# Kernel optimization log

Measured on AMD Instinct MI355X. Metric: run time of the kernel, lower is better.

Reference implementation:

```python
import jax, jax.numpy as jnp
from jax import lax
import numpy as np

BN_EPS = 1e-5

def _bn(x, g, b, m, v):
    # inference-mode BatchNorm1d (running stats)
    return (x - m) * (g / jnp.sqrt(v + BN_EPS)) + b

def _mlp2(x, W1, g, b, m, v, W2):
    # Linear(no bias) -> BN -> ReLU -> (Dropout off in eval) -> Linear(no bias)
    h = jax.nn.relu(_bn(x @ W1.T, g, b, m, v))
    return h @ W2.T

def setup_inputs() -> dict:
    key = jax.random.key(0)
    ks = iter(jax.random.split(key, 40))
    B, N = 1024, 10
    f32 = jnp.float32
    def w(shape, s=0.02):
        return jax.random.normal(next(ks), shape, f32) * s
    def bn_params(c):
        return (jnp.ones((c,), f32), jnp.zeros((c,), f32),
                jax.random.normal(next(ks), (c,), f32) * 0.1,
                jax.random.uniform(next(ks), (c,), f32, 0.5, 1.5))
    inp = {
        'features_object': jax.random.normal(next(ks), (B, N, 1024), f32),
        'bbox': jax.random.uniform(next(ks), (B, N, 4), f32),
        'word_embedding': jax.random.normal(next(ks), (B, N, 300), f32),
        'sentiment': jax.random.normal(next(ks), (B, N, 4096), f32),
        'body': jax.random.normal(next(ks), (B, 2048), f32),
    }
    # mlp_object: 1024 -> 128 -> 128
    inp['W1_o'] = w((128, 1024)); inp['g_o'], inp['b_o'], inp['m_o'], inp['v_o'] = bn_params(128)
    inp['W2_o'] = w((128, 128))
    # mlp_sentiment: 4096 -> 512 -> 128
    inp['W1_s'] = w((512, 4096)); inp['g_s'], inp['b_s'], inp['m_s'], inp['v_s'] = bn_params(512)
    inp['W2_s'] = w((128, 512))
    # mlp_body: 2048 -> 256 -> 128
    inp['W1_b'] = w((256, 2048)); inp['g_b'], inp['b_b'], inp['m_b'], inp['v_b'] = bn_params(256)
    inp['W2_b'] = w((128, 256))
    # channel attention (CBAM-style, in_planes=10, ratio=2): shared MLP 10->5->10
    inp['Wc1'] = w((5, 10), 0.3)
    inp['Wc2'] = w((10, 5), 0.3)
    # spatial attention: Conv1d(2 -> 1, k=7, pad=3, no bias)
    inp['Wsa'] = w((1, 2, 7), 0.3)
    # fc1: 688 -> 256 (with bias) then BN
    inp['Wf'] = w((256, 688)); inp['bf'] = jnp.zeros((256,), f32)
    inp['g_f'], inp['b_f'], inp['m_f'], inp['v_f'] = bn_params(256)
    return inp

def reference(features_object, bbox, word_embedding, sentiment, body,
              W1_o, g_o, b_o, m_o, v_o, W2_o,
              W1_s, g_s, b_s, m_s, v_s, W2_s,
              W1_b, g_b, b_b, m_b, v_b, W2_b,
              Wc1, Wc2, Wsa, Wf, bf, g_f, b_f, m_f, v_f):
    B, N, _ = features_object.shape
    # per-slice MLPs batched into single GEMMs over B*N rows
    obj = _mlp2(features_object.reshape(B * N, -1), W1_o, g_o, b_o, m_o, v_o, W2_o).reshape(B, N, 128)
    sen = _mlp2(sentiment.reshape(B * N, -1), W1_s, g_s, b_s, m_s, v_s, W2_s).reshape(B, N, 128)
    # body is identical across the N repeats (inference BN), compute once and broadcast
    bod = _mlp2(body.reshape(B, -1), W1_b, g_b, b_b, m_b, v_b, W2_b)
    bod = jnp.broadcast_to(bod[:, None, :], (B, N, 128))
    x = jnp.concatenate([obj, bbox, word_embedding, sen, bod], axis=2)  # [B,N,688]
    # channel attention over the N-slice axis
    def ca_mlp(a):  # [B,N] -> [B,N]
        return jax.nn.relu(a @ Wc1.T) @ Wc2.T
    att_c = jax.nn.sigmoid(ca_mlp(x.mean(axis=2)) + ca_mlp(x.max(axis=2)))  # [B,N]
    x = x * att_c[:, :, None]
    # spatial attention along feature axis
    s = jnp.stack([x.mean(axis=1), x.max(axis=1)], axis=1)  # [B,2,688]
    sa = lax.conv_general_dilated(s, Wsa, (1,), [(3, 3)],
                                  dimension_numbers=('NCH', 'OIH', 'NCH'))  # [B,1,688]
    x = x * jax.nn.sigmoid(sa)
    x = x.sum(axis=1)  # [B,688]
    out = jax.nn.relu(_bn(x @ Wf.T + bf, g_f, b_f, m_f, v_f))  # [B,256]
    return out
```

## Files before the change

kernel.cpp:

```cpp
#include <hip/hip_runtime.h>
#include <hip/hip_bf16.h>
#include <math.h>

typedef __attribute__((ext_vector_type(8))) short short8;
typedef __attribute__((ext_vector_type(4))) float floatx4;

static __device__ __forceinline__ unsigned short f2bf(float f) {
    unsigned int u = __float_as_uint(f);
    unsigned int r = (u + 0x7fffu + ((u >> 16) & 1u)) >> 16;
    return (unsigned short)r;
}

static __device__ __forceinline__ void g2l16(const void* g, void* l) {
    __builtin_amdgcn_global_load_lds(
        (const __attribute__((address_space(1))) unsigned int*)g,
        (__attribute__((address_space(3))) unsigned int*)l,
        16, 0, 0);
}

struct GDesc {
    const float*          Af;
    const unsigned short* Ab;
    const unsigned short* W;
    float*          Cf;
    unsigned short* Cb;
    const float *bias, *g, *b, *m, *v;
    int M, N, K;
    int Kreal;
    int fuse;
    int nbx;
    int block0;
};
struct GArgs { GDesc g[3]; int n; };

__global__ __launch_bounds__(256)
void gemm_grouped(GArgs ga)
{
    __shared__ unsigned short As[2][4096];
    __shared__ unsigned short Bs[2][4096];

    const int bid = blockIdx.x;
    int gi = 0;
    #pragma unroll
    for (int i = 1; i < 3; ++i)
        if (i < ga.n && bid >= ga.g[i].block0) gi = i;
    const GDesc d = ga.g[gi];
    const int local = bid - d.block0;
    const int bx = local % d.nbx;
    const int by = local / d.nbx;
    const int row0 = by * 128;
    const int col0 = bx * 128;

    const int tid  = threadIdx.x;
    const int wave = tid >> 6;
    const int lane = tid & 63;
    const int qd   = lane >> 4;
    const int ln   = lane & 15;
    const int wr   = (wave >> 1) * 64;
    const int wc   = (wave & 1) * 64;

    const int c0 = wave * 128 + lane;
    const int c1 = c0 + 64;
    const int r0 = c0 >> 2, k0 = (c0 & 3) * 8;
    const int r1 = c1 >> 2, k1 = (c1 & 3) * 8;

    const int sr = tid >> 3;
    const int sc = (tid & 7) * 4;

    const bool afp = (d.Af != nullptr);
    const int niter = d.K >> 5;

    floatx4 acc[4][4];
    #pragma unroll
    for (int i = 0; i < 4; ++i)
        #pragma unroll
        for (int j = 0; j < 4; ++j) acc[i][j] = (floatx4){0.f, 0.f, 0.f, 0.f};

    g2l16(d.W + (size_t)(col0 + r0) * d.K + k0, &Bs[0][(size_t)wave * 1024]);
    g2l16(d.W + (size_t)(col0 + r1) * d.K + k1, &Bs[0][(size_t)wave * 1024 + 512]);
    if (afp) {
        #pragma unroll
        for (int p = 0; p < 4; ++p) {
            float4 v = (sc < d.Kreal)
                ? *(const float4*)(d.Af + (size_t)(row0 + p * 32 + sr) * d.Kreal + sc)
                : (float4){0.f, 0.f, 0.f, 0.f};
            ushort4 o = { f2bf(v.x), f2bf(v.y), f2bf(v.z), f2bf(v.w) };
            *(ushort4*)&As[0][(p * 32 + sr) * 32 + sc] = o;
        }
    } else {
        g2l16(d.Ab + (size_t)(row0 + r0) * d.K + k0, &As[0][(size_t)wave * 1024]);
        g2l16(d.Ab + (size_t)(row0 + r1) * d.K + k1, &As[0][(size_t)wave * 1024 + 512]);
    }
    __syncthreads();

    int cur = 0;
    for (int it = 0; it < niter; ++it) {
        const int kk = it * 32;
        const int nxt = cur ^ 1;
        const bool pf = (it + 1 < niter);

        float4 areg[4];
        if (pf) {
            const int kn = kk + 32;
            g2l16(d.W + (size_t)(col0 + r0) * d.K + kn + k0, &Bs[nxt][(size_t)wave * 1024]);
            g2l16(d.W + (size_t)(col0 + r1) * d.K + kn + k1, &Bs[nxt][(size_t)wave * 1024 + 512]);
            if (afp) {
                #pragma unroll
                for (int p = 0; p < 4; ++p)
                    areg[p] = (kn + sc < d.Kreal)
                        ? *(const float4*)(d.Af + (size_t)(row0 + p * 32 + sr) * d.Kreal + kn + sc)
                        : (float4){0.f, 0.f, 0.f, 0.f};
            } else {
                g2l16(d.Ab + (size_t)(row0 + r0) * d.K + kn + k0, &As[nxt][(size_t)wave * 1024]);
                g2l16(d.Ab + (size_t)(row0 + r1) * d.K + kn + k1, &As[nxt][(size_t)wave * 1024 + 512]);
            }
        }

        short8 a[4], b[4];
        #pragma unroll
        for (int i = 0; i < 4; ++i)
            a[i] = *(const short8*)&As[cur][(wr + i * 16 + ln) * 32 + qd * 8];
        #pragma unroll
        for (int j = 0; j < 4; ++j)
            b[j] = *(const short8*)&Bs[cur][(wc + j * 16 + ln) * 32 + qd * 8];
        #pragma unroll
        for (int i = 0; i < 4; ++i)
            #pragma unroll
            for (int j = 0; j < 4; ++j)
                acc[i][j] = __builtin_amdgcn_mfma_f32_16x16x32_bf16(
                                a[i], b[j], acc[i][j], 0, 0, 0);

        if (pf && afp) {
            #pragma unroll
            for (int p = 0; p < 4; ++p) {
                ushort4 o = { f2bf(areg[p].x), f2bf(areg[p].y),
                              f2bf(areg[p].z), f2bf(areg[p].w) };
                *(ushort4*)&As[nxt][(p * 32 + sr) * 32 + sc] = o;
            }
        }
        __syncthreads();
        cur = nxt;
    }

    #pragma unroll
    for (int j = 0; j < 4; ++j) {
        const int col = col0 + wc + j * 16 + ln;
        float add = d.bias ? d.bias[col] : 0.f;
        float scale = 1.f, shift = 0.f;
        if (d.fuse) {
            scale = d.g[col] * rsqrtf(d.v[col] + 1e-5f);
            shift = d.b[col] - d.m[col] * scale;
        }
        #pragma unroll
        for (int i = 0; i < 4; ++i) {
            #pragma unroll
            for (int r = 0; r < 4; ++r) {
                const int row = row0 + wr + i * 16 + qd * 4 + r;
                float vv = acc[i][j][r] + add;
                if (d.fuse) vv = fmaxf(vv * scale + shift, 0.f);
                if (d.Cf) d.Cf[(size_t)row * d.N + col] = vv;
                if (d.Cb) d.Cb[(size_t)row * d.N + col] = f2bf(vv);
            }
        }
    }
}

struct WSeg { const float* src; unsigned short* dst; int Kreal; int Kp; };
struct WArgs { WSeg s[7]; int off[8]; };

__global__ __launch_bounds__(256)
void cvt_weights(WArgs wa)
{
    int i = blockIdx.x * 256 + threadIdx.x;
    if (i >= wa.off[7]) return;
    int s = 0;
    #pragma unroll
    for (int j = 1; j < 7; ++j) if (i >= wa.off[j]) s = j;
    const WSeg sg = wa.s[s];
    const int li = i - wa.off[s];
    const int r = li / sg.Kp, c = li - r * sg.Kp;
    sg.dst[li] = (c < sg.Kreal) ? f2bf(sg.src[(size_t)r * sg.Kreal + c])
                                : (unsigned short)0;
}

__global__ __launch_bounds__(256)
void attn_kernel(const float* __restrict__ obj, const float* __restrict__ bbox,
                 const float* __restrict__ word, const float* __restrict__ sen,
                 const float* __restrict__ bod,
                 const float* __restrict__ Wc1, const float* __restrict__ Wc2,
                 const float* __restrict__ Wsa,
                 float* __restrict__ xsum_out)
{
    const int b = blockIdx.x;
    const int tid = threadIdx.x;

    __shared__ float xs[10][688];
    __shared__ float s0[688], s1[688];
    __shared__ float avec[10], mvec[10], att[10];
    __shared__ float cw[14], c1[50], c2[50];

    if (tid < 14) cw[tid] = Wsa[tid];
    if (tid < 50) { c1[tid] = Wc1[tid]; c2[tid] = Wc2[tid]; }

    for (int n = 0; n < 10; ++n) {
        const float* o  = obj  + ((size_t)b * 10 + n) * 128;
        const float* bx = bbox + ((size_t)b * 10 + n) * 4;
        const float* w  = word + ((size_t)b * 10 + n) * 300;
        const float* s  = sen  + ((size_t)b * 10 + n) * 128;
        const float* bo = bod  + (size_t)b * 128;
        for (int c = tid; c < 688; c += 256) {
            float v;
            if      (c < 128) v = o[c];
            else if (c < 132) v = bx[c - 128];
            else if (c < 432) v = w[c - 132];
            else if (c < 560) v = s[c - 432];
            else              v = bo[c - 560];
            xs[n][c] = v;
        }
    }
    __syncthreads();

    if (tid < 10) {
        float sm = 0.f, mx = -INFINITY;
        for (int c = 0; c < 688; ++c) {
            float v = xs[tid][c];
            sm += v; mx = fmaxf(mx, v);
        }
        avec[tid] = sm * (1.f / 688.f);
        mvec[tid] = mx;
    }
    __syncthreads();

    if (tid == 0) {
        float ha[5], hm[5];
        #pragma unroll
        for (int i = 0; i < 5; ++i) {
            float sa_ = 0.f, sm_ = 0.f;
            #pragma unroll
            for (int j = 0; j < 10; ++j) {
                sa_ += c1[i * 10 + j] * avec[j];
                sm_ += c1[i * 10 + j] * mvec[j];
            }
            ha[i] = fmaxf(sa_, 0.f);
            hm[i] = fmaxf(sm_, 0.f);
        }
        #pragma unroll
        for (int j = 0; j < 10; ++j) {
            float v = 0.f;
            #pragma unroll
            for (int i = 0; i < 5; ++i) v += c2[j * 5 + i] * (ha[i] + hm[i]);
            att[j] = 1.f / (1.f + expf(-v));
        }
    }
    __syncthreads();

    for (int c = tid; c < 688; c += 256) {
        float sm = 0.f, mx = -INFINITY;
        #pragma unroll
        for (int n = 0; n < 10; ++n) {
            float v = xs[n][c] * att[n];
            xs[n][c] = v;
            sm += v; mx = fmaxf(mx, v);
        }
        s0[c] = sm * 0.1f;
        s1[c] = mx;
    }
    __syncthreads();

    for (int c = tid; c < 688; c += 256) {
        float sa = 0.f;
        #pragma unroll
        for (int j = 0; j < 7; ++j) {
            int cc = c + j - 3;
            if (cc >= 0 && cc < 688)
                sa += cw[j] * s0[cc] + cw[7 + j] * s1[cc];
        }
        float sig = 1.f / (1.f + expf(-sa));
        float sm = 0.f;
        #pragma unroll
        for (int n = 0; n < 10; ++n) sm += xs[n][c];
        xsum_out[(size_t)b * 688 + c] = sm * sig;
    }
}

extern "C" void kernel_launch(void* const* d_in, const int* in_sizes, int n_in,
                              void* d_out, int out_size, void* d_ws, size_t ws_size,
                              hipStream_t stream)
{
    const float* f_obj = (const float*)d_in[0];
    const float* bbox  = (const float*)d_in[1];
    const float* word  = (const float*)d_in[2];
    const float* sent  = (const float*)d_in[3];
    const float* body  = (const float*)d_in[4];
    const float* W1_o  = (const float*)d_in[5];
    const float* g_o = (const float*)d_in[6],  *b_o = (const float*)d_in[7];
    const float* m_o = (const float*)d_in[8],  *v_o = (const float*)d_in[9];
    const float* W2_o  = (const float*)d_in[10];
    const float* W1_s  = (const float*)d_in[11];
    const float* g_s = (const float*)d_in[12], *b_s = (const float*)d_in[13];
    const float* m_s = (const float*)d_in[14], *v_s = (const float*)d_in[15];
    const float* W2_s  = (const float*)d_in[16];
    const float* W1_b  = (const float*)d_in[17];
    const float* g_b = (const float*)d_in[18], *b_b = (const float*)d_in[19];
    const float* m_b = (const float*)d_in[20], *v_b = (const float*)d_in[21];
    const float* W2_b  = (const float*)d_in[22];
    const float* Wc1 = (const float*)d_in[23];
    const float* Wc2 = (const float*)d_in[24];
    const float* Wsa = (const float*)d_in[25];
    const float* Wf  = (const float*)d_in[26];
    const float* bf  = (const float*)d_in[27];
    const float* g_f = (const float*)d_in[28], *b_f = (const float*)d_in[29];
    const float* m_f = (const float*)d_in[30], *v_f = (const float*)d_in[31];
    float* out = (float*)d_out;

    char* p = (char*)d_ws;
    unsigned short* w1s = (unsigned short*)p; p += 4194304;
    unsigned short* w2s = (unsigned short*)p; p += 131072;
    unsigned short* w1o = (unsigned short*)p; p += 262144;
    unsigned short* w2o = (unsigned short*)p; p += 32768;
    unsigned short* w1b = (unsigned short*)p; p += 1048576;
    unsigned short* w2b = (unsigned short*)p; p += 65536;
    unsigned short* wfp = (unsigned short*)p; p += 360448;
    unsigned short* h_s = (unsigned short*)p; p += 10485760;
    unsigned short* h_o = (unsigned short*)p; p += 2621440;
    unsigned short* h_b = (unsigned short*)p; p += 524288;
    float* sen_f  = (float*)p; p += 5242880;
    float* obj_f  = (float*)p; p += 5242880;
    float* bod_f  = (float*)p; p += 524288;
    float* xsum_f = (float*)p; p += 2818048;
    if ((size_t)(p - (char*)d_ws) > ws_size) return;

    WArgs wa;
    wa.s[0] = { W1_s, w1s, 4096, 4096 };
    wa.s[1] = { W2_s, w2s,  512,  512 };
    wa.s[2] = { W1_o, w1o, 1024, 1024 };
    wa.s[3] = { W2_o, w2o,  128,  128 };
    wa.s[4] = { W1_b, w1b, 2048, 2048 };
    wa.s[5] = { W2_b, w2b,  256,  256 };
    wa.s[6] = { Wf,   wfp,  688,  704 };
    const int wn[7] = { 512*4096, 128*512, 128*1024, 128*128, 256*2048, 128*256, 256*704 };
    wa.off[0] = 0;
    for (int i = 0; i < 7; ++i) wa.off[i + 1] = wa.off[i] + wn[i];
    cvt_weights<<<(wa.off[7] + 255) / 256, 256, 0, stream>>>(wa);

    {
        GArgs ga; ga.n = 3;
        ga.g[0] = { sent,  nullptr, w1s, nullptr, h_s, nullptr, g_s, b_s, m_s, v_s,
                    10240, 512, 4096, 4096, 1, 4, 0 };
        ga.g[1] = { f_obj, nullptr, w1o, nullptr, h_o, nullptr, g_o, b_o, m_o, v_o,
                    10240, 128, 1024, 1024, 1, 1, 320 };
        ga.g[2] = { body,  nullptr, w1b, nullptr, h_b, nullptr, g_b, b_b, m_b, v_b,
                    1024, 256, 2048, 2048, 1, 2, 400 };
        gemm_grouped<<<416, 256, 0, stream>>>(ga);
    }

    {
        GArgs ga; ga.n = 3;
        ga.g[0] = { nullptr, h_s, w2s, sen_f, nullptr, nullptr, nullptr, nullptr, nullptr, nullptr,
                    10240, 128, 512, 512, 0, 1, 0 };
        ga.g[1] = { nullptr, h_o, w2o, obj_f, nullptr, nullptr, nullptr, nullptr, nullptr, nullptr,
                    10240, 128, 128, 128, 0, 1, 80 };
        ga.g[2] = { nullptr, h_b, w2b, bod_f, nullptr, nullptr, nullptr, nullptr, nullptr, nullptr,
                    1024, 128, 256, 256, 0, 1, 160 };
        gemm_grouped<<<168, 256, 0, stream>>>(ga);
    }

    attn_kernel<<<1024, 256, 0, stream>>>(obj_f, bbox, word, sen_f, bod_f,
                                          Wc1, Wc2, Wsa, xsum_f);

    {
        GArgs ga; ga.n = 1;
        ga.g[0] = { xsum_f, nullptr, wfp, out, nullptr, bf, g_f, b_f, m_f, v_f,
                    1024, 256, 704, 688, 1, 2, 0 };
        gemm_grouped<<<16, 256, 0, stream>>>(ga);
    }
}
```

Before: 539.0 us.

## Register-staged two-deep GEMM pipeline, XCD swizzle, bf16 intermediates, parallel attention reductions

Replaces the direct global-to-LDS loads with register-staged loads that prefetch two K-steps ahead, so global latency overlaps with MFMA work. Adds an XCD-aware block swizzle for the large sentiment GEMM to improve L2 reuse of A rows. Second-layer GEMM outputs are now stored as bf16 instead of fp32, halving intermediate traffic, and the attention kernel reads them as bf16. The per-slice mean and max reductions are spread across wave lanes with shuffle reductions instead of running on ten serial threads. The costs are higher register pressure, reduced precision of the intermediates, and a swizzle that assumes a fixed 8-way XCD layout.

```diff
diff --git a/kernel.cpp b/kernel.cpp
--- a/kernel.cpp
+++ b/kernel.cpp
@@ -10,12 +10,8 @@
     unsigned int r = (u + 0x7fffu + ((u >> 16) & 1u)) >> 16;
     return (unsigned short)r;
 }
-
-static __device__ __forceinline__ void g2l16(const void* g, void* l) {
-    __builtin_amdgcn_global_load_lds(
-        (const __attribute__((address_space(1))) unsigned int*)g,
-        (__attribute__((address_space(3))) unsigned int*)l,
-        16, 0, 0);
+static __device__ __forceinline__ float bf2f(unsigned short h) {
+    return __uint_as_float(((unsigned int)h) << 16);
 }
 
 struct GDesc {
@@ -30,11 +26,12 @@
     int fuse;
     int nbx;
     int block0;
+    int swz;
 };
 struct GArgs { GDesc g[3]; int n; };
 
 __global__ __launch_bounds__(256)
-void gemm_grouped(GArgs ga)
+void gemm_pipe(GArgs ga)
 {
     __shared__ unsigned short As[2][4096];
     __shared__ unsigned short Bs[2][4096];
@@ -46,8 +43,15 @@
         if (i < ga.n && bid >= ga.g[i].block0) gi = i;
     const GDesc d = ga.g[gi];
     const int local = bid - d.block0;
-    const int bx = local % d.nbx;
-    const int by = local / d.nbx;
+    int bx, by;
+    if (d.swz) {
+        const int xcd = local & 7, t = local >> 3;
+        bx = t & 3;
+        by = (t >> 2) * 8 + xcd;
+    } else {
+        bx = local % d.nbx;
+        by = local / d.nbx;
+    }
     const int row0 = by * 128;
     const int col0 = bx * 128;
 
@@ -59,16 +63,59 @@
     const int wr   = (wave >> 1) * 64;
     const int wc   = (wave & 1) * 64;
 
-    const int c0 = wave * 128 + lane;
-    const int c1 = c0 + 64;
-    const int r0 = c0 >> 2, k0 = (c0 & 3) * 8;
-    const int r1 = c1 >> 2, k1 = (c1 & 3) * 8;
-
-    const int sr = tid >> 3;
-    const int sc = (tid & 7) * 4;
+    const int r0  = tid >> 2;
+    const int ko0 = (tid & 3) * 8;
+    const int r1  = r0 + 64;
 
     const bool afp = (d.Af != nullptr);
-    const int niter = d.K >> 5;
+    const int T = d.K >> 5;
+
+    float4 fa[2][4];
+    uint4  ba[2][2];
+    uint4  bb[2][2];
+
+    auto LOAD = [&](int s, int kk) {
+        if (afp) {
+            if (kk + ko0 < d.Kreal) {
+                const float* p0 = d.Af + (size_t)(row0 + r0) * d.Kreal + kk + ko0;
+                fa[s][0] = *(const float4*)p0;
+                fa[s][1] = *(const float4*)(p0 + 4);
+            } else {
+                fa[s][0] = fa[s][1] = (float4){0.f, 0.f, 0.f, 0.f};
+            }
+            if (kk + ko0 < d.Kreal) {
+                const float* p1 = d.Af + (size_t)(row0 + r1) * d.Kreal + kk + ko0;
+                fa[s][2] = *(const float4*)p1;
+                fa[s][3] = *(const float4*)(p1 + 4);
+            } else {
+                fa[s][2] = fa[s][3] = (float4){0.f, 0.f, 0.f, 0.f};
+            }
+        } else {
+            ba[s][0] = *(const uint4*)(d.Ab + (size_t)(row0 + r0) * d.K + kk + ko0);
+            ba[s][1] = *(const uint4*)(d.Ab + (size_t)(row0 + r1) * d.K + kk + ko0);
+        }
+        bb[s][0] = *(const uint4*)(d.W + (size_t)(col0 + r0) * d.K + kk + ko0);
+        bb[s][1] = *(const uint4*)(d.W + (size_t)(col0 + r1) * d.K + kk + ko0);
+    };
+    auto PACK = [&](const float4& lo, const float4& hi) -> uint4 {
+        uint4 pk;
+        pk.x = f2bf(lo.x) | ((unsigned)f2bf(lo.y) << 16);
+        pk.y = f2bf(lo.z) | ((unsigned)f2bf(lo.w) << 16);
+        pk.z = f2bf(hi.x) | ((unsigned)f2bf(hi.y) << 16);
+        pk.w = f2bf(hi.z) | ((unsigned)f2bf(hi.w) << 16);
+        return pk;
+    };
+    auto STORE = [&](int s, int buf) {
+        if (afp) {
+            *(uint4*)&As[buf][tid * 8]        = PACK(fa[s][0], fa[s][1]);
+            *(uint4*)&As[buf][tid * 8 + 2048] = PACK(fa[s][2], fa[s][3]);
+        } else {
+            *(uint4*)&As[buf][tid * 8]        = ba[s][0];
+            *(uint4*)&As[buf][tid * 8 + 2048] = ba[s][1];
+        }
+        *(uint4*)&Bs[buf][tid * 8]        = bb[s][0];
+        *(uint4*)&Bs[buf][tid * 8 + 2048] = bb[s][1];
+    };
 
     floatx4 acc[4][4];
     #pragma unroll
@@ -76,45 +123,14 @@
         #pragma unroll
         for (int j = 0; j < 4; ++j) acc[i][j] = (floatx4){0.f, 0.f, 0.f, 0.f};
 
-    g2l16(d.W + (size_t)(col0 + r0) * d.K + k0, &Bs[0][(size_t)wave * 1024]);
-    g2l16(d.W + (size_t)(col0 + r1) * d.K + k1, &Bs[0][(size_t)wave * 1024 + 512]);
-    if (afp) {
-        #pragma unroll
-        for (int p = 0; p < 4; ++p) {
-            float4 v = (sc < d.Kreal)
-                ? *(const float4*)(d.Af + (size_t)(row0 + p * 32 + sr) * d.Kreal + sc)
-                : (float4){0.f, 0.f, 0.f, 0.f};
-            ushort4 o = { f2bf(v.x), f2bf(v.y), f2bf(v.z), f2bf(v.w) };
-            *(ushort4*)&As[0][(p * 32 + sr) * 32 + sc] = o;
-        }
-    } else {
-        g2l16(d.Ab + (size_t)(row0 + r0) * d.K + k0, &As[0][(size_t)wave * 1024]);
-        g2l16(d.Ab + (size_t)(row0 + r1) * d.K + k1, &As[0][(size_t)wave * 1024 + 512]);
-    }
+    LOAD(0, 0);
+    if (T > 1) LOAD(1, 32);
+    STORE(0, 0);
     __syncthreads();
 
     int cur = 0;
-    for (int it = 0; it < niter; ++it) {
-        const int kk = it * 32;
-        const int nxt = cur ^ 1;
-        const bool pf = (it + 1 < niter);
-
-        float4 areg[4];
-        if (pf) {
-            const int kn = kk + 32;
-            g2l16(d.W + (size_t)(col0 + r0) * d.K + kn + k0, &Bs[nxt][(size_t)wave * 1024]);
-            g2l16(d.W + (size_t)(col0 + r1) * d.K + kn + k1, &Bs[nxt][(size_t)wave * 1024 + 512]);
-            if (afp) {
-                #pragma unroll
-                for (int p = 0; p < 4; ++p)
-                    areg[p] = (kn + sc < d.Kreal)
-                        ? *(const float4*)(d.Af + (size_t)(row0 + p * 32 + sr) * d.Kreal + kn + sc)
-                        : (float4){0.f, 0.f, 0.f, 0.f};
-            } else {
-                g2l16(d.Ab + (size_t)(row0 + r0) * d.K + kn + k0, &As[nxt][(size_t)wave * 1024]);
-                g2l16(d.Ab + (size_t)(row0 + r1) * d.K + kn + k1, &As[nxt][(size_t)wave * 1024 + 512]);
-            }
-        }
+    for (int it = 0; it < T; ++it) {
+        if (it + 2 < T) LOAD(it & 1, (it + 2) * 32);
 
         short8 a[4], b[4];
         #pragma unroll
@@ -130,16 +146,9 @@
                 acc[i][j] = __builtin_amdgcn_mfma_f32_16x16x32_bf16(
                                 a[i], b[j], acc[i][j], 0, 0, 0);
 
-        if (pf && afp) {
-            #pragma unroll
-            for (int p = 0; p < 4; ++p) {
-                ushort4 o = { f2bf(areg[p].x), f2bf(areg[p].y),
-                              f2bf(areg[p].z), f2bf(areg[p].w) };
-                *(ushort4*)&As[nxt][(p * 32 + sr) * 32 + sc] = o;
-            }
-        }
+        if (it + 1 < T) STORE((it + 1) & 1, cur ^ 1);
         __syncthreads();
-        cur = nxt;
+        cur ^= 1;
     }
 
     #pragma unroll
@@ -184,15 +193,19 @@
 }
 
 __global__ __launch_bounds__(256)
-void attn_kernel(const float* __restrict__ obj, const float* __restrict__ bbox,
-                 const float* __restrict__ word, const float* __restrict__ sen,
-                 const float* __restrict__ bod,
+void attn_kernel(const unsigned short* __restrict__ obj,
+                 const float* __restrict__ bbox,
+                 const float* __restrict__ word,
+                 const unsigned short* __restrict__ sen,
+                 const unsigned short* __restrict__ bod,
                  const float* __restrict__ Wc1, const float* __restrict__ Wc2,
                  const float* __restrict__ Wsa,
                  float* __restrict__ xsum_out)
 {
     const int b = blockIdx.x;
     const int tid = threadIdx.x;
+    const int wave = tid >> 6;
+    const int lane = tid & 63;
 
     __shared__ float xs[10][688];
     __shared__ float s0[688], s1[688];
@@ -203,31 +216,35 @@
     if (tid < 50) { c1[tid] = Wc1[tid]; c2[tid] = Wc2[tid]; }
 
     for (int n = 0; n < 10; ++n) {
-        const float* o  = obj  + ((size_t)b * 10 + n) * 128;
+        const unsigned short* o = obj + ((size_t)b * 10 + n) * 128;
         const float* bx = bbox + ((size_t)b * 10 + n) * 4;
         const float* w  = word + ((size_t)b * 10 + n) * 300;
-        const float* s  = sen  + ((size_t)b * 10 + n) * 128;
-        const float* bo = bod  + (size_t)b * 128;
+        const unsigned short* s = sen + ((size_t)b * 10 + n) * 128;
+        const unsigned short* bo = bod + (size_t)b * 128;
         for (int c = tid; c < 688; c += 256) {
             float v;
-            if      (c < 128) v = o[c];
+            if      (c < 128) v = bf2f(o[c]);
             else if (c < 132) v = bx[c - 128];
             else if (c < 432) v = w[c - 132];
-            else if (c < 560) v = s[c - 432];
-            else              v = bo[c - 560];
+            else if (c < 560) v = bf2f(s[c - 432]);
+            else              v = bf2f(bo[c - 560]);
             xs[n][c] = v;
         }
     }
     __syncthreads();
 
-    if (tid < 10) {
+    for (int n = wave; n < 10; n += 4) {
         float sm = 0.f, mx = -INFINITY;
-        for (int c = 0; c < 688; ++c) {
-            float v = xs[tid][c];
+        for (int c = lane; c < 688; c += 64) {
+            float v = xs[n][c];
             sm += v; mx = fmaxf(mx, v);
         }
-        avec[tid] = sm * (1.f / 688.f);
-        mvec[tid] = mx;
+        #pragma unroll
+        for (int off = 32; off > 0; off >>= 1) {
+            sm += __shfl_down(sm, off);
+            mx = fmaxf(mx, __shfl_down(mx, off));
+        }
+        if (lane == 0) { avec[n] = sm * (1.f / 688.f); mvec[n] = mx; }
     }
     __syncthreads();
 
@@ -324,9 +341,9 @@
     unsigned short* h_s = (unsigned short*)p; p += 10485760;
     unsigned short* h_o = (unsigned short*)p; p += 2621440;
     unsigned short* h_b = (unsigned short*)p; p += 524288;
-    float* sen_f  = (float*)p; p += 5242880;
-    float* obj_f  = (float*)p; p += 5242880;
-    float* bod_f  = (float*)p; p += 524288;
+    unsigned short* sen_b = (unsigned short*)p; p += 2621440;
+    unsigned short* obj_b = (unsigned short*)p; p += 2621440;
+    unsigned short* bod_b = (unsigned short*)p; p += 262144;
     float* xsum_f = (float*)p; p += 2818048;
     if ((size_t)(p - (char*)d_ws) > ws_size) return;
 
@@ -346,32 +363,32 @@
     {
         GArgs ga; ga.n = 3;
         ga.g[0] = { sent,  nullptr, w1s, nullptr, h_s, nullptr, g_s, b_s, m_s, v_s,
-                    10240, 512, 4096, 4096, 1, 4, 0 };
+                    10240, 512, 4096, 4096, 1, 4, 0, 1 };
         ga.g[1] = { f_obj, nullptr, w1o, nullptr, h_o, nullptr, g_o, b_o, m_o, v_o,
-                    10240, 128, 1024, 1024, 1, 1, 320 };
+                    10240, 128, 1024, 1024, 1, 1, 320, 0 };
         ga.g[2] = { body,  nullptr, w1b, nullptr, h_b, nullptr, g_b, b_b, m_b, v_b,
-                    1024, 256, 2048, 2048, 1, 2, 400 };
-        gemm_grouped<<<416, 256, 0, stream>>>(ga);
+                    1024, 256, 2048, 2048, 1, 2, 400, 0 };
+        gemm_pipe<<<416, 256, 0, stream>>>(ga);
     }
 
     {
         GArgs ga; ga.n = 3;
-        ga.g[0] = { nullptr, h_s, w2s, sen_f, nullptr, nullptr, nullptr, nullptr, nullptr, nullptr,
-                    10240, 128, 512, 512, 0, 1, 0 };
-        ga.g[1] = { nullptr, h_o, w2o, obj_f, nullptr, nullptr, nullptr, nullptr, nullptr, nullptr,
-                    10240, 128, 128, 128, 0, 1, 80 };
-        ga.g[2] = { nullptr, h_b, w2b, bod_f, nullptr, nullptr, nullptr, nullptr, nullptr, nullptr,
-                    1024, 128, 256, 256, 0, 1, 160 };
-        gemm_grouped<<<168, 256, 0, stream>>>(ga);
-    }
-
-    attn_kernel<<<1024, 256, 0, stream>>>(obj_f, bbox, word, sen_f, bod_f,
+        ga.g[0] = { nullptr, h_s, w2s, nullptr, sen_b, nullptr, nullptr, nullptr, nullptr, nullptr,
+                    10240, 128, 512, 512, 0, 1, 0, 0 };
+        ga.g[1] = { nullptr, h_o, w2o, nullptr, obj_b, nullptr, nullptr, nullptr, nullptr, nullptr,
+                    10240, 128, 128, 128, 0, 1, 80, 0 };
+        ga.g[2] = { nullptr, h_b, w2b, nullptr, bod_b, nullptr, nullptr, nullptr, nullptr, nullptr,
+                    1024, 128, 256, 256, 0, 1, 160, 0 };
+        gemm_pipe<<<168, 256, 0, stream>>>(ga);
+    }
+
+    attn_kernel<<<1024, 256, 0, stream>>>(obj_b, bbox, word, sen_b, bod_b,
                                           Wc1, Wc2, Wsa, xsum_f);
 
     {
         GArgs ga; ga.n = 1;
         ga.g[0] = { xsum_f, nullptr, wfp, out, nullptr, bf, g_f, b_f, m_f, v_f,
-                    1024, 256, 704, 688, 1, 2, 0 };
-        gemm_grouped<<<16, 256, 0, stream>>>(ga);
-    }
-}
+                    1024, 256, 704, 688, 1, 2, 0, 0 };
+        gemm_pipe<<<16, 256, 0, stream>>>(ga);
+    }
+}
```

After: 1.008 ms. 1.87x slower.
